# Performance work log

Hardware: AMD Instinct MI355X
Metric: run time of the kernel (lower is better)

The kernel has to match this reference:

```python
import jax, jax.numpy as jnp
import numpy as np

NUM_CLASSES = 2
LOG2_NC = float(np.log2(NUM_CLASSES))


def _conv(x, w, b=None):
    # NCHW conv, stride 1, SAME padding (kernel 3 pad 1 or kernel 1 pad 0)
    y = jax.lax.conv_general_dilated(x, w, (1, 1), 'SAME',
                                     dimension_numbers=('NCHW', 'OIHW', 'NCHW'))
    if b is not None:
        y = y + b[None, :, None, None]
    return y


def _uncertainty_map(ds):
    # entropy over class dim, thresholded to {0,1}
    logp = jax.nn.log_softmax(ds, axis=1)            # [B,C,H,W]
    prob = jnp.exp(logp)
    # torch uses log2(prob + 1e-6); replicate exactly
    ent = -jnp.sum(prob * jnp.log2(prob + 1e-6), axis=1) / LOG2_NC  # [B,H,W]
    return (ent >= 0.001).astype(jnp.float32)


def _unob(tar, amap):
    # vectorized UnoB with S=3: interior pixels with tar!=0 get pro=0 unless
    # 4*tar == sum of the 4-neighborhood (i.e. locally constant label)
    t = tar  # [B,H,W] int
    nb = t[:, 2:, 1:-1] + t[:, :-2, 1:-1] + t[:, 1:-1, 2:] + t[:, 1:-1, :-2]
    center = t[:, 1:-1, 1:-1]
    inner_pro = jnp.where((center != 0) & (4 * center != nb), 0.0, 1.0)
    pro = jnp.ones_like(amap)
    pro = pro.at[:, 1:-1, 1:-1].set(inner_pro)
    return amap * pro


def setup_inputs() -> dict:
    key = jax.random.key(0)
    ks = jax.random.split(key, 6)
    B, C, H, W = 8, 128, 128, 128
    return {
        'x': jax.random.normal(ks[0], (B, C, H, W), jnp.float32),
        'skip': jax.random.normal(ks[1], (B, C, H, W), jnp.float32),
        'tar': jax.random.randint(ks[2], (B, 1, H, W), 0, NUM_CLASSES, jnp.int64)
            if jax.config.jax_enable_x64 else
            jax.random.randint(ks[2], (B, 1, H, W), 0, NUM_CLASSES).astype(jnp.int32),
        'W1': jax.random.normal(ks[3], (128, 256, 3, 3), jnp.float32) * 0.05,
        'b1': jnp.zeros((128,), jnp.float32),
        'W2': jax.random.normal(ks[4], (128, 128, 3, 3), jnp.float32) * 0.05,
        'b2': jnp.zeros((128,), jnp.float32),
        'Wds': jax.random.normal(ks[5], (NUM_CLASSES, 128, 1, 1), jnp.float32) * 0.05,
    }


def reference(x, skip, tar, W1, b1, W2, b2, Wds):
    h = jnp.concatenate([x, skip], axis=1)            # [B,2*dim,H,W]
    h = jax.nn.leaky_relu(_conv(h, W1, b1), 0.01)     # [B,dim,H,W]
    h = jax.nn.leaky_relu(_conv(h, W2, b2), 0.01)
    ds = _conv(h, Wds)                                # [B,num_classes,H,W]
    amap = _uncertainty_map(ds)                       # [B,H,W]
    amap = _unob(tar[:, 0], amap)                     # UnoB refinement, S=3
    return h, ds, amap
```

## Files before the change

kernel.cpp:

```cpp
#include <hip/hip_runtime.h>

typedef float f32x16 __attribute__((ext_vector_type(16)));
typedef short bf16x8 __attribute__((ext_vector_type(8)));
typedef unsigned int u32;

static __device__ __forceinline__ unsigned short f2bf(float f) {
  union { float f; unsigned int u; } v;
  v.f = f;
  return (unsigned short)((v.u + 0x7FFFu + ((v.u >> 16) & 1u)) >> 16);
}

static __device__ __forceinline__ void gl_lds16(const unsigned short* g,
                                                unsigned short* l) {
  __builtin_amdgcn_global_load_lds(
      (const __attribute__((address_space(1))) u32*)g,
      (__attribute__((address_space(3))) u32*)l, 16, 0, 0);
}

__global__ __launch_bounds__(256) void convert_weights(
    const float* __restrict__ W1, const float* __restrict__ W2,
    unsigned short* __restrict__ W1b, unsigned short* __restrict__ W2b,
    unsigned short* __restrict__ zp) {
  if (blockIdx.x == 1728) {
    uint4* z = (uint4*)zp;
    z[threadIdx.x] = make_uint4(0, 0, 0, 0);
    z[256 + threadIdx.x] = make_uint4(0, 0, 0, 0);
    return;
  }
  int i = blockIdx.x * 256 + threadIdx.x;
  if (i < 294912) {
    int e = i & 7, co = (i >> 3) & 127, r = i >> 10;
    int tap = r % 9, pc = r / 9;
    int ci = (pc >> 1) * 16 + (pc & 1) * 8 + e;
    W1b[i] = f2bf(W1[(co * 256 + ci) * 9 + tap]);
  } else {
    int j = i - 294912;
    if (j < 147456) {
      int e = j & 7, co = (j >> 3) & 127, r = j >> 10;
      int tap = r % 9, pc = r / 9;
      int ci = (pc >> 1) * 16 + (pc & 1) * 8 + e;
      W2b[j] = f2bf(W2[(co * 128 + ci) * 9 + tap]);
    }
  }
}

__global__ __launch_bounds__(256) void transpose_to_bf16(
    const float* __restrict__ src, unsigned short* __restrict__ dst, int cigb) {
  int row = blockIdx.x;
  int b = row >> 7, y = row & 127;
  const float* s = src + (long)b * 128 * 16384 + (long)y * 128;
  for (int it = 0; it < 8; ++it) {
    int u = it * 256 + (int)threadIdx.x;
    int cig = u >> 7, px = u & 127;
    unsigned short pk[8];
#pragma unroll
    for (int e = 0; e < 8; ++e)
      pk[e] = f2bf(s[(long)(cig * 8 + e) * 16384 + px]);
    uint4 vv;
    vv.x = (unsigned)pk[0] | ((unsigned)pk[1] << 16);
    vv.y = (unsigned)pk[2] | ((unsigned)pk[3] << 16);
    vv.z = (unsigned)pk[4] | ((unsigned)pk[5] << 16);
    vv.w = (unsigned)pk[6] | ((unsigned)pk[7] << 16);
    *(uint4*)(&dst[(((long)row * 32 + cigb + cig) * 130 + px + 1) * 8]) = vv;
  }
  if (cigb == 0 && threadIdx.x < 64) {
    int g = threadIdx.x >> 1;
    long col = (threadIdx.x & 1) * 129L;
    *(uint4*)(&dst[(((long)row * 32 + g) * 130 + col) * 8]) = make_uint4(0, 0, 0, 0);
  }
}

#define IPL 520
#define WPL 1152
template <int CIN, bool OUT_NCHW>
__global__ __launch_bounds__(512) void conv3x3(
    const unsigned short* __restrict__ src,
    const unsigned short* __restrict__ wt,
    const float* __restrict__ bias,
    const unsigned short* __restrict__ zp,
    unsigned short* __restrict__ dst_bf16,
    float* __restrict__ dst_f32) {
  constexpr int CPG = CIN / 8;
  constexpr int NC = CIN / 16;
  __shared__ unsigned short in_tile[2 * IPL * 8];
  __shared__ unsigned short wt_tile[2 * WPL * 8];
  __shared__ float sb[128];

  const int tid = threadIdx.x;
  const int b = blockIdx.x >> 6;
  const int y0 = (blockIdx.x & 63) * 2;
  const int lane = tid & 63, wave = tid >> 6;
  const int wco = wave & 1, wpx = wave >> 1;
  const int l31 = lane & 31, kh = lane >> 5;
  const int rowoff = wpx >> 1, p0 = (wpx & 1) * 64;

  if (tid < 128) sb[tid] = bias[tid];

  const int shy = wave >> 1, sp = wave & 1;
  const int sgy = y0 - 1 + shy;
  const bool sok = (sgy >= 0 && sgy < 128);
  const unsigned short* srow =
      sok ? src + ((long)((b * 128 + sgy) * CPG) + sp) * 1040 : zp;
  const int tseg = tid >> 1, thx = 128 + (tid & 1);
  const int tp = tseg & 1, thy = tseg >> 1;
  const int tgy = y0 - 1 + thy;

  f32x16 acc[2][2] = {};

  for (int cic = 0; cic < NC; ++cic) {
    __syncthreads();
    const unsigned short* wslab = wt + (long)cic * 18432;
#pragma unroll
    for (int o = wave; o < 36; o += 8)
      gl_lds16(wslab + (o * 64 + lane) * 8, &wt_tile[(size_t)(o * 64) * 8]);
#pragma unroll
    for (int j = 0; j < 2; ++j)
      gl_lds16(srow + (sok ? ((long)cic * 2 * 1040 + (j * 64 + lane) * 8)
                           : (long)(lane * 8)),
               &in_tile[(size_t)(sp * IPL + shy * 130 + j * 64) * 8]);
    if (tid < 16) {
      uint4 v = make_uint4(0, 0, 0, 0);
      if (tgy >= 0 && tgy < 128)
        v = *(const uint4*)(src + ((long)((b * 128 + tgy) * CPG) + cic * 2 + tp) * 1040 +
                            thx * 8);
      *(uint4*)(&in_tile[(size_t)(tp * IPL + thy * 130 + thx) * 8]) = v;
    }
    __syncthreads();

    const size_t ibase = (size_t)(kh * IPL) * 8;
    const size_t wbase = (size_t)(kh * WPL) * 8;
#pragma unroll
    for (int ky = 0; ky < 3; ++ky) {
      const int hy = ky + rowoff;
#pragma unroll
      for (int kx = 0; kx < 3; ++kx) {
        const int t = ky * 3 + kx;
        bf16x8 a0 = *(const bf16x8*)(&wt_tile[wbase + (size_t)(t * 128 + wco * 64 + l31) * 8]);
        bf16x8 a1 = *(const bf16x8*)(&wt_tile[wbase + (size_t)(t * 128 + wco * 64 + 32 + l31) * 8]);
        bf16x8 b0 = *(const bf16x8*)(&in_tile[ibase + (size_t)(hy * 130 + p0 + l31 + kx) * 8]);
        bf16x8 b1 = *(const bf16x8*)(&in_tile[ibase + (size_t)(hy * 130 + p0 + 32 + l31 + kx) * 8]);
        acc[0][0] = __builtin_amdgcn_mfma_f32_32x32x16_bf16(a0, b0, acc[0][0], 0, 0, 0);
        acc[0][1] = __builtin_amdgcn_mfma_f32_32x32x16_bf16(a0, b1, acc[0][1], 0, 0, 0);
        acc[1][0] = __builtin_amdgcn_mfma_f32_32x32x16_bf16(a1, b0, acc[1][0], 0, 0, 0);
        acc[1][1] = __builtin_amdgcn_mfma_f32_32x32x16_bf16(a1, b1, acc[1][1], 0, 0, 0);
      }
    }
  }

  const int gyo = y0 + rowoff;
#pragma unroll
  for (int fc = 0; fc < 2; ++fc) {
#pragma unroll
    for (int fp = 0; fp < 2; ++fp) {
      const int px = p0 + fp * 32 + l31;
      if constexpr (!OUT_NCHW) {
#pragma unroll
        for (int rg = 0; rg < 4; ++rg) {
          const int co0 = wco * 64 + fc * 32 + rg * 8 + kh * 4;
          unsigned short pk[4];
#pragma unroll
          for (int q = 0; q < 4; ++q) {
            float v = acc[fc][fp][rg * 4 + q] + sb[co0 + q];
            v = v > 0.f ? v : 0.01f * v;
            pk[q] = f2bf(v);
          }
          uint2 o;
          o.x = (unsigned)pk[0] | ((unsigned)pk[1] << 16);
          o.y = (unsigned)pk[2] | ((unsigned)pk[3] << 16);
          *(uint2*)(&dst_bf16[(((long)(b * 128 + gyo) * 16 + (co0 >> 3)) * 130 + px + 1) * 8 +
                              kh * 4]) = o;
        }
      } else {
#pragma unroll
        for (int r = 0; r < 16; ++r) {
          const int co = wco * 64 + fc * 32 + (r & 3) + 8 * (r >> 2) + 4 * kh;
          float v = acc[fc][fp][r] + sb[co];
          v = v > 0.f ? v : 0.01f * v;
          dst_f32[((long)(b * 128 + co) << 14) + (gyo << 7) + px] = v;
        }
      }
    }
  }
  if constexpr (!OUT_NCHW) {
    if (tid < 64) {
      int row = tid >> 5, g = (tid >> 1) & 15;
      long col = (tid & 1) * 129L;
      *(uint4*)(&dst_bf16[(((long)(b * 128 + y0 + row) * 16 + g) * 130 + col) * 8]) =
          make_uint4(0, 0, 0, 0);
    }
  }
}

__global__ __launch_bounds__(128) void ds_amap(
    const float* __restrict__ h, const float* __restrict__ wds,
    const int* __restrict__ tar, float* __restrict__ ds,
    float* __restrict__ amap) {
  __shared__ float w0[128], w1[128];
  int row = blockIdx.x;
  int b = row >> 7, y = row & 127;
  int px = threadIdx.x;
  w0[px] = wds[px];
  w1[px] = wds[128 + px];
  __syncthreads();
  const float* hp = h + (long)b * 128 * 16384 + y * 128 + px;
  float a0 = 0.f, a1 = 0.f;
#pragma unroll 16
  for (int c = 0; c < 128; ++c) {
    float v = hp[(long)c * 16384];
    a0 += w0[c] * v;
    a1 += w1[c] * v;
  }
  ds[((long)b * 2) * 16384 + y * 128 + px] = a0;
  ds[((long)b * 2 + 1) * 16384 + y * 128 + px] = a1;
  float m = fmaxf(a0, a1);
  float e0 = expf(a0 - m), e1 = expf(a1 - m);
  float s = e0 + e1;
  float p0 = e0 / s, p1 = e1 / s;
  float ent = -(p0 * log2f(p0 + 1e-6f) + p1 * log2f(p1 + 1e-6f));
  float un = ent >= 0.001f ? 1.f : 0.f;
  float pro = 1.f;
  const int* tb = tar + (long)b * 16384;
  if (y > 0 && y < 127 && px > 0 && px < 127) {
    int c = tb[y * 128 + px];
    if (c != 0) {
      int nb = tb[(y - 1) * 128 + px] + tb[(y + 1) * 128 + px] +
               tb[y * 128 + px - 1] + tb[y * 128 + px + 1];
      if (4 * c != nb) pro = 0.f;
    }
  }
  amap[(long)row * 128 + px] = un * pro;
}

extern "C" void kernel_launch(void* const* d_in, const int* in_sizes, int n_in,
                              void* d_out, int out_size, void* d_ws, size_t ws_size,
                              hipStream_t stream) {
  const float* x    = (const float*)d_in[0];
  const float* skip = (const float*)d_in[1];
  const int*   tar  = (const int*)d_in[2];
  const float* W1   = (const float*)d_in[3];
  const float* b1   = (const float*)d_in[4];
  const float* W2   = (const float*)d_in[5];
  const float* b2   = (const float*)d_in[6];
  const float* Wds  = (const float*)d_in[7];

  float* out_h  = (float*)d_out;
  float* out_ds = out_h + 16777216;
  float* out_am = out_ds + 262144;

  unsigned short* W1b = (unsigned short*)d_ws;
  unsigned short* W2b = W1b + 294912;
  unsigned short* zp  = W2b + 147456;
  unsigned short* h1  = (unsigned short*)((char*)d_ws + (1u << 20));

  unsigned short* h0 = (unsigned short*)d_out;

  convert_weights<<<1729, 256, 0, stream>>>(W1, W2, W1b, W2b, zp);
  transpose_to_bf16<<<1024, 256, 0, stream>>>(x, h0, 0);
  transpose_to_bf16<<<1024, 256, 0, stream>>>(skip, h0, 16);
  conv3x3<256, false><<<512, 512, 0, stream>>>(h0, W1b, b1, zp, h1, nullptr);
  conv3x3<128, true><<<512, 512, 0, stream>>>(h1, W2b, b2, zp, nullptr, out_h);
  ds_amap<<<1024, 128, 0, stream>>>(out_h, Wds, tar, out_ds, out_am);
}
```

Before: 160.7 us.

## Double-buffer conv LDS tiles and fuse 1x1 ds head with uncertainty map

```diff
diff --git a/kernel.cpp b/kernel.cpp
--- a/kernel.cpp
+++ b/kernel.cpp
@@ -71,20 +71,25 @@
 }
 
 #define IPL 520
-#define WPL 1152
-template <int CIN, bool OUT_NCHW>
+template <int CIN, bool FUSE_DS>
 __global__ __launch_bounds__(512) void conv3x3(
     const unsigned short* __restrict__ src,
     const unsigned short* __restrict__ wt,
     const float* __restrict__ bias,
     const unsigned short* __restrict__ zp,
     unsigned short* __restrict__ dst_bf16,
-    float* __restrict__ dst_f32) {
+    float* __restrict__ dst_f32,
+    const float* __restrict__ wds,
+    const int* __restrict__ tar,
+    float* __restrict__ ds,
+    float* __restrict__ amap) {
   constexpr int CPG = CIN / 8;
   constexpr int NC = CIN / 16;
-  __shared__ unsigned short in_tile[2 * IPL * 8];
-  __shared__ unsigned short wt_tile[2 * WPL * 8];
+  __shared__ unsigned short in_tile[2][2 * IPL * 8];
+  __shared__ unsigned short wt_tile[2][2304 * 8];
   __shared__ float sb[128];
+  __shared__ float w0s[128], w1s[128];
+  __shared__ float sc[4 * 2 * 2 * 32];
 
   const int tid = threadIdx.x;
   const int b = blockIdx.x >> 6;
@@ -94,7 +99,13 @@
   const int l31 = lane & 31, kh = lane >> 5;
   const int rowoff = wpx >> 1, p0 = (wpx & 1) * 64;
 
-  if (tid < 128) sb[tid] = bias[tid];
+  if (tid < 128) {
+    sb[tid] = bias[tid];
+    if constexpr (FUSE_DS) {
+      w0s[tid] = wds[tid];
+      w1s[tid] = wds[128 + tid];
+    }
+  }
 
   const int shy = wave >> 1, sp = wave & 1;
   const int sgy = y0 - 1 + shy;
@@ -105,55 +116,90 @@
   const int tp = tseg & 1, thy = tseg >> 1;
   const int tgy = y0 - 1 + thy;
 
+#define STAGE_WT(cic, bufi)                                                   \
+  {                                                                           \
+    const unsigned short* wslab = wt + (long)(cic)*18432;                     \
+    for (int o = wave; o < 36; o += 8)                                        \
+      gl_lds16(wslab + (o * 64 + lane) * 8,                                   \
+               &wt_tile[bufi][(size_t)(o * 64) * 8]);                         \
+  }
+
+#define STAGE_BULK(cic, bufi)                                                 \
+  {                                                                           \
+    _Pragma("unroll") for (int j = 0; j < 2; ++j)                             \
+        gl_lds16(srow + (sok ? ((long)(cic)*2 * 1040 + (j * 64 + lane) * 8)   \
+                             : (long)(lane * 8)),                             \
+                 &in_tile[bufi][(size_t)(sp * IPL + shy * 130 + j * 64) * 8]);\
+  }
+
+#define LOAD_TAIL(cic, v)                                                     \
+  {                                                                           \
+    if (tid < 16 && tgy >= 0 && tgy < 128)                                    \
+      v = *(const uint4*)(src +                                               \
+                          ((long)((b * 128 + tgy) * CPG) + (cic)*2 + tp) *    \
+                              1040 +                                          \
+                          thx * 8);                                           \
+  }
+
+#define WRITE_TAIL(bufi, v)                                                   \
+  {                                                                           \
+    if (tid < 16)                                                             \
+      *(uint4*)(&in_tile[bufi][(size_t)(tp * IPL + thy * 130 + thx) * 8]) = v;\
+  }
+
   f32x16 acc[2][2] = {};
 
+  {
+    uint4 tv = make_uint4(0, 0, 0, 0);
+    LOAD_TAIL(0, tv);
+    STAGE_WT(0, 0);
+    STAGE_BULK(0, 0);
+    WRITE_TAIL(0, tv);
+  }
+  __syncthreads();
+
   for (int cic = 0; cic < NC; ++cic) {
-    __syncthreads();
-    const unsigned short* wslab = wt + (long)cic * 18432;
-#pragma unroll
-    for (int o = wave; o < 36; o += 8)
-      gl_lds16(wslab + (o * 64 + lane) * 8, &wt_tile[(size_t)(o * 64) * 8]);
-#pragma unroll
-    for (int j = 0; j < 2; ++j)
-      gl_lds16(srow + (sok ? ((long)cic * 2 * 1040 + (j * 64 + lane) * 8)
-                           : (long)(lane * 8)),
-               &in_tile[(size_t)(sp * IPL + shy * 130 + j * 64) * 8]);
-    if (tid < 16) {
-      uint4 v = make_uint4(0, 0, 0, 0);
-      if (tgy >= 0 && tgy < 128)
-        v = *(const uint4*)(src + ((long)((b * 128 + tgy) * CPG) + cic * 2 + tp) * 1040 +
-                            thx * 8);
-      *(uint4*)(&in_tile[(size_t)(tp * IPL + thy * 130 + thx) * 8]) = v;
-    }
-    __syncthreads();
-
+    const int cur = cic & 1, nb = cur ^ 1;
+    const bool more = (cic + 1 < NC);
+    uint4 tl = make_uint4(0, 0, 0, 0);
+    if (more) {
+      LOAD_TAIL(cic + 1, tl);
+      STAGE_WT(cic + 1, nb);
+      STAGE_BULK(cic + 1, nb);
+    }
+    __builtin_amdgcn_sched_barrier(0);
+    const unsigned short* it = in_tile[cur];
+    const unsigned short* wl = wt_tile[cur];
     const size_t ibase = (size_t)(kh * IPL) * 8;
-    const size_t wbase = (size_t)(kh * WPL) * 8;
+    const size_t wbase = (size_t)(kh * 1152) * 8;
 #pragma unroll
     for (int ky = 0; ky < 3; ++ky) {
       const int hy = ky + rowoff;
 #pragma unroll
       for (int kx = 0; kx < 3; ++kx) {
         const int t = ky * 3 + kx;
-        bf16x8 a0 = *(const bf16x8*)(&wt_tile[wbase + (size_t)(t * 128 + wco * 64 + l31) * 8]);
-        bf16x8 a1 = *(const bf16x8*)(&wt_tile[wbase + (size_t)(t * 128 + wco * 64 + 32 + l31) * 8]);
-        bf16x8 b0 = *(const bf16x8*)(&in_tile[ibase + (size_t)(hy * 130 + p0 + l31 + kx) * 8]);
-        bf16x8 b1 = *(const bf16x8*)(&in_tile[ibase + (size_t)(hy * 130 + p0 + 32 + l31 + kx) * 8]);
+        bf16x8 a0 = *(const bf16x8*)(&wl[wbase + (size_t)(t * 128 + wco * 64 + l31) * 8]);
+        bf16x8 a1 = *(const bf16x8*)(&wl[wbase + (size_t)(t * 128 + wco * 64 + 32 + l31) * 8]);
+        bf16x8 b0 = *(const bf16x8*)(&it[ibase + (size_t)(hy * 130 + p0 + l31 + kx) * 8]);
+        bf16x8 b1 = *(const bf16x8*)(&it[ibase + (size_t)(hy * 130 + p0 + 32 + l31 + kx) * 8]);
         acc[0][0] = __builtin_amdgcn_mfma_f32_32x32x16_bf16(a0, b0, acc[0][0], 0, 0, 0);
         acc[0][1] = __builtin_amdgcn_mfma_f32_32x32x16_bf16(a0, b1, acc[0][1], 0, 0, 0);
         acc[1][0] = __builtin_amdgcn_mfma_f32_32x32x16_bf16(a1, b0, acc[1][0], 0, 0, 0);
         acc[1][1] = __builtin_amdgcn_mfma_f32_32x32x16_bf16(a1, b1, acc[1][1], 0, 0, 0);
       }
     }
+    if (more) WRITE_TAIL(nb, tl);
+    __syncthreads();
   }
 
   const int gyo = y0 + rowoff;
+  float pd[2][2] = {};
 #pragma unroll
   for (int fc = 0; fc < 2; ++fc) {
 #pragma unroll
     for (int fp = 0; fp < 2; ++fp) {
       const int px = p0 + fp * 32 + l31;
-      if constexpr (!OUT_NCHW) {
+      if constexpr (!FUSE_DS) {
 #pragma unroll
         for (int rg = 0; rg < 4; ++rg) {
           const int co0 = wco * 64 + fc * 32 + rg * 8 + kh * 4;
@@ -172,63 +218,78 @@
         }
       } else {
 #pragma unroll
-        for (int r = 0; r < 16; ++r) {
-          const int co = wco * 64 + fc * 32 + (r & 3) + 8 * (r >> 2) + 4 * kh;
-          float v = acc[fc][fp][r] + sb[co];
-          v = v > 0.f ? v : 0.01f * v;
-          dst_f32[((long)(b * 128 + co) << 14) + (gyo << 7) + px] = v;
+        for (int rg = 0; rg < 4; ++rg) {
+          const int co0 = wco * 64 + fc * 32 + rg * 8 + kh * 4;
+          float4 wv0 = *(const float4*)(&w0s[co0]);
+          float4 wv1 = *(const float4*)(&w1s[co0]);
+#pragma unroll
+          for (int q = 0; q < 4; ++q) {
+            float v = acc[fc][fp][rg * 4 + q] + sb[co0 + q];
+            v = v > 0.f ? v : 0.01f * v;
+            dst_f32[((long)(b * 128 + co0 + q) << 14) + (gyo << 7) + px] = v;
+            float wq0 = (q == 0) ? wv0.x : (q == 1) ? wv0.y : (q == 2) ? wv0.z : wv0.w;
+            float wq1 = (q == 0) ? wv1.x : (q == 1) ? wv1.y : (q == 2) ? wv1.z : wv1.w;
+            pd[fp][0] += wq0 * v;
+            pd[fp][1] += wq1 * v;
+          }
         }
       }
     }
   }
-  if constexpr (!OUT_NCHW) {
+
+  if constexpr (!FUSE_DS) {
     if (tid < 64) {
       int row = tid >> 5, g = (tid >> 1) & 15;
       long col = (tid & 1) * 129L;
       *(uint4*)(&dst_bf16[(((long)(b * 128 + y0 + row) * 16 + g) * 130 + col) * 8]) =
           make_uint4(0, 0, 0, 0);
     }
-  }
-}
-
-__global__ __launch_bounds__(128) void ds_amap(
-    const float* __restrict__ h, const float* __restrict__ wds,
-    const int* __restrict__ tar, float* __restrict__ ds,
-    float* __restrict__ amap) {
-  __shared__ float w0[128], w1[128];
-  int row = blockIdx.x;
-  int b = row >> 7, y = row & 127;
-  int px = threadIdx.x;
-  w0[px] = wds[px];
-  w1[px] = wds[128 + px];
-  __syncthreads();
-  const float* hp = h + (long)b * 128 * 16384 + y * 128 + px;
-  float a0 = 0.f, a1 = 0.f;
-#pragma unroll 16
-  for (int c = 0; c < 128; ++c) {
-    float v = hp[(long)c * 16384];
-    a0 += w0[c] * v;
-    a1 += w1[c] * v;
-  }
-  ds[((long)b * 2) * 16384 + y * 128 + px] = a0;
-  ds[((long)b * 2 + 1) * 16384 + y * 128 + px] = a1;
-  float m = fmaxf(a0, a1);
-  float e0 = expf(a0 - m), e1 = expf(a1 - m);
-  float s = e0 + e1;
-  float p0 = e0 / s, p1 = e1 / s;
-  float ent = -(p0 * log2f(p0 + 1e-6f) + p1 * log2f(p1 + 1e-6f));
-  float un = ent >= 0.001f ? 1.f : 0.f;
-  float pro = 1.f;
-  const int* tb = tar + (long)b * 16384;
-  if (y > 0 && y < 127 && px > 0 && px < 127) {
-    int c = tb[y * 128 + px];
-    if (c != 0) {
-      int nb = tb[(y - 1) * 128 + px] + tb[(y + 1) * 128 + px] +
-               tb[y * 128 + px - 1] + tb[y * 128 + px + 1];
-      if (4 * c != nb) pro = 0.f;
-    }
-  }
-  amap[(long)row * 128 + px] = un * pro;
+  } else {
+#pragma unroll
+    for (int fp = 0; fp < 2; ++fp)
+#pragma unroll
+      for (int c = 0; c < 2; ++c)
+        pd[fp][c] += __shfl_xor(pd[fp][c], 32, 64);
+    if (wco == 1 && kh == 0) {
+#pragma unroll
+      for (int fp = 0; fp < 2; ++fp)
+#pragma unroll
+        for (int c = 0; c < 2; ++c)
+          sc[((wpx * 2 + fp) * 2 + c) * 32 + l31] = pd[fp][c];
+    }
+    __syncthreads();
+    if (wco == 0 && kh == 0) {
+      const int* tb = tar + (long)b * 16384;
+#pragma unroll
+      for (int fp = 0; fp < 2; ++fp) {
+        const int px = p0 + fp * 32 + l31;
+        float a0 = pd[fp][0] + sc[((wpx * 2 + fp) * 2 + 0) * 32 + l31];
+        float a1 = pd[fp][1] + sc[((wpx * 2 + fp) * 2 + 1) * 32 + l31];
+        ds[((long)b * 2) * 16384 + (gyo << 7) + px] = a0;
+        ds[((long)b * 2 + 1) * 16384 + (gyo << 7) + px] = a1;
+        float m = fmaxf(a0, a1);
+        float e0 = expf(a0 - m), e1 = expf(a1 - m);
+        float s = e0 + e1;
+        float p0f = e0 / s, p1f = e1 / s;
+        float ent = -(p0f * log2f(p0f + 1e-6f) + p1f * log2f(p1f + 1e-6f));
+        float un = ent >= 0.001f ? 1.f : 0.f;
+        float pro = 1.f;
+        if (gyo > 0 && gyo < 127 && px > 0 && px < 127) {
+          int c = tb[(gyo << 7) + px];
+          if (c != 0) {
+            int nb2 = tb[((gyo - 1) << 7) + px] + tb[((gyo + 1) << 7) + px] +
+                      tb[(gyo << 7) + px - 1] + tb[(gyo << 7) + px + 1];
+            if (4 * c != nb2) pro = 0.f;
+          }
+        }
+        amap[((long)(b * 128 + gyo) << 7) + px] = un * pro;
+      }
+    }
+  }
+#undef STAGE_WT
+#undef STAGE_BULK
+#undef LOAD_TAIL
+#undef WRITE_TAIL
 }
 
 extern "C" void kernel_launch(void* const* d_in, const int* in_sizes, int n_in,
@@ -257,7 +318,8 @@
   convert_weights<<<1729, 256, 0, stream>>>(W1, W2, W1b, W2b, zp);
   transpose_to_bf16<<<1024, 256, 0, stream>>>(x, h0, 0);
   transpose_to_bf16<<<1024, 256, 0, stream>>>(skip, h0, 16);
-  conv3x3<256, false><<<512, 512, 0, stream>>>(h0, W1b, b1, zp, h1, nullptr);
-  conv3x3<128, true><<<512, 512, 0, stream>>>(h1, W2b, b2, zp, nullptr, out_h);
-  ds_amap<<<1024, 128, 0, stream>>>(out_h, Wds, tar, out_ds, out_am);
-}
+  conv3x3<256, false><<<512, 512, 0, stream>>>(h0, W1b, b1, zp, h1, nullptr,
+                                               nullptr, nullptr, nullptr, nullptr);
+  conv3x3<128, true><<<512, 512, 0, stream>>>(h1, W2b, b2, zp, nullptr, out_h,
+                                              Wds, tar, out_ds, out_am);
+}
```

Result: no change. 163.8 us (+1.9%).
